# Kernel tuning notes

Hardware: AMD Instinct MI355X
Metric: run time of the kernel (lower is better)

The kernel has to match this reference:

```python
import jax, jax.numpy as jnp
import numpy as np

EMBED = 256      # input_size
DOWN = 64        # expert hidden_size
NUM_EXPERTS = 10
TOPK = 2
GATE_SCALE = 0.5
LOSS_COEF = 1.0
CV_EPS = 1e-10


def setup_inputs() -> dict:
    key = jax.random.key(0)
    ks = jax.random.split(key, 6)
    B, N = 16, 4096
    x = jax.random.normal(ks[0], (B, N, EMBED), jnp.float32)
    # gating weight (Parameter in torch; random here so top-k is non-degenerate)
    w_gate = jax.random.normal(ks[1], (EMBED, NUM_EXPERTS), jnp.float32) * 0.02
    # expert MLP params: fc1 (EMBED->DOWN), relu, fc2 (DOWN->EMBED)
    w1 = jax.random.normal(ks[2], (NUM_EXPERTS, EMBED, DOWN), jnp.float32) * (1.0 / np.sqrt(EMBED))
    b1 = jnp.zeros((NUM_EXPERTS, DOWN), jnp.float32)
    w2 = jax.random.normal(ks[3], (NUM_EXPERTS, DOWN, EMBED), jnp.float32) * (1.0 / np.sqrt(DOWN))
    b2 = jnp.zeros((NUM_EXPERTS, EMBED), jnp.float32)
    return {"x": x, "w_gate": w_gate, "w1": w1, "b1": b1, "w2": w2, "b2": b2}


def _cv_squared(v):
    # torch: x.var() / (x.mean()**2 + eps), unbiased variance
    return jnp.var(v, ddof=1) / (jnp.mean(v) ** 2 + CV_EPS)


def reference(x, w_gate, w1, b1, w2, b2):
    B, N, D = x.shape
    xt = x.reshape(B * N, D)                      # (T, D)
    T = B * N

    # --- noisy top-k gating (eval mode: no noise) ---
    logits = xt @ w_gate                          # (T, E)
    top_logits, top_idx = jax.lax.top_k(logits, TOPK)
    top_gates = jax.nn.softmax(top_logits, axis=-1)
    gates = jnp.zeros((T, NUM_EXPERTS), x.dtype).at[
        jnp.arange(T)[:, None], top_idx].set(top_gates)   # (T, E), sparse rows

    importance = gates.sum(axis=0)                               # (E,)
    load = jnp.sum(gates > 0, axis=0).astype(x.dtype)            # (E,)
    aux_loss = (_cv_squared(importance) + _cv_squared(load)) * LOSS_COEF

    # --- expert FFN dispatch+combine (dense equivalent: zero gates kill terms) ---
    h = jax.nn.relu(jnp.einsum('td,edh->teh', xt, w1) + b1[None])   # (T, E, DOWN)
    ye = jnp.einsum('teh,eho->teo', h, w2) + b2[None]               # (T, E, D)
    y = jnp.einsum('te,teo->to', gates, ye)                         # (T, D)

    out = y.reshape(B, N, -1)
    # self-KD L1 loss vs zeros, computed BEFORE gate_scale is applied
    kd_loss = jnp.mean(jnp.abs(out))
    moe_loss = aux_loss + kd_loss
    return out * GATE_SCALE, moe_loss
```

## Files before the change

### kernel.cpp

```cpp
#include <hip/hip_runtime.h>
#include <hip/hip_bf16.h>

#define T_TOKENS 65536
#define EMBED 256
#define DOWN 64
#define NE 10
#define NPAIR 100
#define MAXQ 1280
#define XROW 72

typedef __attribute__((ext_vector_type(8))) short short8;
typedef __attribute__((ext_vector_type(4))) float f32x4;

__device__ inline unsigned short f2bf(float f) {
    unsigned u = __builtin_bit_cast(unsigned, f);
    u += 0x7fff + ((u >> 16) & 1);
    return (unsigned short)(u >> 16);
}
__device__ inline float bf2f(unsigned short h) {
    unsigned u = ((unsigned)h) << 16;
    return __builtin_bit_cast(float, u);
}

__global__ __launch_bounds__(256) void pack_kernel(
    const float* __restrict__ w1, const float* __restrict__ w2,
    unsigned short* __restrict__ w1ph, unsigned short* __restrict__ w1pl,
    unsigned short* __restrict__ w2ph, unsigned short* __restrict__ w2pl)
{
    int gid = blockIdx.x * 256 + threadIdx.x;
    int lane = gid & 63;
    int fid = gid >> 6;
    int n16 = lane & 15;
    int kbase = ((lane >> 4) & 3) * 8;
    if (fid < 320) {
        int kb = fid & 7, ect = fid >> 3;
        int ct = ect & 3, e = ect >> 2;
        int n = ct * 16 + n16;
        int k0 = kb * 32 + kbase;
#pragma unroll
        for (int j = 0; j < 8; ++j) {
            float v = w1[((size_t)e * EMBED + k0 + j) * DOWN + n];
            unsigned short h = f2bf(v);
            w1ph[(size_t)fid * 512 + lane * 8 + j] = h;
            w1pl[(size_t)fid * 512 + lane * 8 + j] = f2bf(v - bf2f(h));
        }
    } else if (fid < 640) {
        int f2 = fid - 320;
        int kb = f2 & 1, ect = f2 >> 1;
        int ct = ect & 15, e = ect >> 4;
        int n = ct * 16 + n16;
        int k0 = kb * 32 + kbase;
#pragma unroll
        for (int j = 0; j < 8; ++j) {
            float v = w2[((size_t)e * DOWN + k0 + j) * EMBED + n];
            unsigned short h = f2bf(v);
            w2ph[(size_t)f2 * 512 + lane * 8 + j] = h;
            w2pl[(size_t)f2 * 512 + lane * 8 + j] = f2bf(v - bf2f(h));
        }
    }
}

__global__ __launch_bounds__(256) void gating_kernel(
    const float* __restrict__ x, const float* __restrict__ wg,
    int* __restrict__ pcount, float* __restrict__ importance,
    int* __restrict__ btok, float* __restrict__ bg0)
{
    __shared__ float Xs[2][256 * 33];
    __shared__ int lcount[NPAIR];
    __shared__ int gbase[NPAIR];
    __shared__ float limp[16];
    int tid = threadIdx.x;
    if (tid < NPAIR) lcount[tid] = 0;
    if (tid < 16) limp[tid] = 0.f;

    int tokbase = blockIdx.x * 256;
    const float4* x4 = (const float4*)x;
    int rbase = tid >> 3, c4 = tid & 7;

    float4 pre0[8], pre1[8];
#pragma unroll
    for (int i = 0; i < 8; ++i)
        pre0[i] = x4[(size_t)(tokbase + i * 32 + rbase) * 64 + c4];
#pragma unroll
    for (int i = 0; i < 8; ++i)
        pre1[i] = x4[(size_t)(tokbase + i * 32 + rbase) * 64 + 8 + c4];

    float acc[NE];
#pragma unroll
    for (int e = 0; e < NE; e++) acc[e] = 0.f;

    for (int cp = 0; cp < 4; ++cp) {
        {
            float* buf = Xs[0];
#pragma unroll
            for (int i = 0; i < 8; ++i) {
                float* d = &buf[(i * 32 + rbase) * 33 + c4 * 4];
                d[0] = pre0[i].x; d[1] = pre0[i].y; d[2] = pre0[i].z; d[3] = pre0[i].w;
            }
            if (cp < 3) {
#pragma unroll
                for (int i = 0; i < 8; ++i)
                    pre0[i] = x4[(size_t)(tokbase + i * 32 + rbase) * 64 + (2 * cp + 2) * 8 + c4];
            }
            __syncthreads();
            const float* wgc = wg + (2 * cp) * 32 * NE;
#pragma unroll
            for (int c = 0; c < 32; ++c) {
                float xv = buf[tid * 33 + c];
#pragma unroll
                for (int e = 0; e < NE; ++e)
                    acc[e] = fmaf(xv, wgc[c * NE + e], acc[e]);
            }
        }
        {
            float* buf = Xs[1];
#pragma unroll
            for (int i = 0; i < 8; ++i) {
                float* d = &buf[(i * 32 + rbase) * 33 + c4 * 4];
                d[0] = pre1[i].x; d[1] = pre1[i].y; d[2] = pre1[i].z; d[3] = pre1[i].w;
            }
            if (cp < 3) {
#pragma unroll
                for (int i = 0; i < 8; ++i)
                    pre1[i] = x4[(size_t)(tokbase + i * 32 + rbase) * 64 + (2 * cp + 3) * 8 + c4];
            }
            __syncthreads();
            const float* wgc = wg + (2 * cp + 1) * 32 * NE;
#pragma unroll
            for (int c = 0; c < 32; ++c) {
                float xv = buf[tid * 33 + c];
#pragma unroll
                for (int e = 0; e < NE; ++e)
                    acc[e] = fmaf(xv, wgc[c * NE + e], acc[e]);
            }
        }
    }

    float l0 = -INFINITY, l1 = -INFINITY;
    int i0 = 0, i1 = 0;
#pragma unroll
    for (int e = 0; e < NE; e++) {
        float v = acc[e];
        if (v > l0) { l1 = l0; i1 = i0; l0 = v; i0 = e; }
        else if (v > l1) { l1 = v; i1 = e; }
    }
    float ex = __expf(l1 - l0);
    float g0 = 1.f / (1.f + ex);

    int p = i0 * NE + i1;
    int lp = atomicAdd(&lcount[p], 1);
    atomicAdd(&limp[i0], g0);
    atomicAdd(&limp[i1], 1.f - g0);
    __syncthreads();
    if (tid < NPAIR) {
        int c = lcount[tid];
        gbase[tid] = c ? atomicAdd(&pcount[tid], c) : 0;
    }
    if (tid < NE) atomicAdd(&importance[tid], limp[tid]);
    __syncthreads();
    int pos = gbase[p] + lp;
    btok[p * T_TOKENS + pos] = tokbase + tid;
    bg0[p * T_TOKENS + pos] = g0;
}

__global__ __launch_bounds__(128) void queue_kernel(const int* __restrict__ pcount,
                             int* __restrict__ qp, int* __restrict__ qs, int* __restrict__ nq)
{
    __shared__ int sc[2][128];
    int tid = threadIdx.x;
    int c = (tid < NPAIR) ? pcount[tid] : 0;
    int t = (c + 63) >> 6;
    sc[0][tid] = t;
    __syncthreads();
    int cur = 0;
#pragma unroll
    for (int o = 1; o < 128; o <<= 1) {
        int v = sc[cur][tid] + ((tid >= o) ? sc[cur][tid - o] : 0);
        sc[cur ^ 1][tid] = v;
        __syncthreads();
        cur ^= 1;
    }
    int incl = sc[cur][tid];
    int excl = incl - t;
    if (tid == 127) *nq = incl;
    for (int i = 0; i < t; ++i) { qp[excl + i] = tid; qs[excl + i] = i * 64; }
}

__global__ __launch_bounds__(256, 3) void expert_kernel(
    const float* __restrict__ x,
    const unsigned short* __restrict__ w1ph, const unsigned short* __restrict__ w1pl,
    const unsigned short* __restrict__ w2ph, const unsigned short* __restrict__ w2pl,
    const float* __restrict__ b1, const float* __restrict__ b2,
    const int* __restrict__ pcount, const int* __restrict__ qp, const int* __restrict__ qs,
    const int* __restrict__ nq,
    const int* __restrict__ btok, const float* __restrict__ bg0,
    float* __restrict__ out, float* __restrict__ kdpart)
{
    int bid = blockIdx.x;
    if (bid >= *nq) return;
    int p = qp[bid], s = qs[bid];
    int e0 = p / NE, e1 = p - e0 * NE;
    int m = min(64, pcount[p] - s);

    __shared__ __align__(16) unsigned short Hbuf[16384];
    __shared__ int toks[64];
    __shared__ float gv0s[64], gv1s[64];
    __shared__ float kdw[4];

    unsigned short* const Xh  = Hbuf;
    unsigned short* const Xl  = Hbuf + 64 * XROW;
    unsigned short* const H0h = Hbuf;
    unsigned short* const H0l = Hbuf + 4096;
    unsigned short* const H1h = Hbuf + 8192;
    unsigned short* const H1l = Hbuf + 12288;

    int tid = threadIdx.x;
    if (tid < 64) {
        int v = 0; float g = 0.f;
        if (tid < m) {
            v = btok[p * T_TOKENS + s + tid];
            g = bg0[p * T_TOKENS + s + tid];
        }
        toks[tid] = v;
        gv0s[tid] = g;
        gv1s[tid] = (tid < m) ? (1.f - g) : 0.f;
    }
    __syncthreads();

    int lane = tid & 63, wv = tid >> 6;
    int ln15 = lane & 15, quad = lane >> 4;
    int srow = tid >> 2, sc0 = (tid & 3) * 16;
    const float* xrow = x + (size_t)toks[srow] * EMBED;
    bool srow_ok = srow < m;

    f32x4 a10[4], a11[4];
#pragma unroll
    for (int rt = 0; rt < 4; ++rt) { a10[rt] = (f32x4){0,0,0,0}; a11[rt] = (f32x4){0,0,0,0}; }

    const unsigned short* w1h0 = w1ph + (((size_t)e0 * 4 + wv) * 8) * 512;
    const unsigned short* w1l0 = w1pl + (((size_t)e0 * 4 + wv) * 8) * 512;
    const unsigned short* w1h1 = w1ph + (((size_t)e1 * 4 + wv) * 8) * 512;
    const unsigned short* w1l1 = w1pl + (((size_t)e1 * 4 + wv) * 8) * 512;

    for (int cc = 0; cc < 4; ++cc) {
#pragma unroll
        for (int p4 = 0; p4 < 4; ++p4) {
            int col = sc0 + p4 * 4;
            float4 v = make_float4(0.f, 0.f, 0.f, 0.f);
            if (srow_ok) v = *(const float4*)(xrow + cc * 64 + col);
            const float* vs = (const float*)&v;
            ushort4 hv, lv;
            unsigned short* hp = (unsigned short*)&hv;
            unsigned short* lp2 = (unsigned short*)&lv;
#pragma unroll
            for (int i = 0; i < 4; ++i) {
                unsigned short h = f2bf(vs[i]);
                hp[i] = h;
                lp2[i] = f2bf(vs[i] - bf2f(h));
            }
            *(ushort4*)&Xh[srow * XROW + col] = hv;
            *(ushort4*)&Xl[srow * XROW + col] = lv;
        }
        __syncthreads();
#pragma unroll
        for (int kb = 0; kb < 2; ++kb) {
            int kbg = cc * 2 + kb;
            short8 bh0 = *(const short8*)(w1h0 + (size_t)kbg * 512 + lane * 8);
            short8 bl0 = *(const short8*)(w1l0 + (size_t)kbg * 512 + lane * 8);
            short8 bh1 = *(const short8*)(w1h1 + (size_t)kbg * 512 + lane * 8);
            short8 bl1 = *(const short8*)(w1l1 + (size_t)kbg * 512 + lane * 8);
            int aoff = kb * 32 + quad * 8;
#pragma unroll
            for (int rt = 0; rt < 4; ++rt) {
                short8 ah = *(const short8*)&Xh[(rt * 16 + ln15) * XROW + aoff];
                short8 al = *(const short8*)&Xl[(rt * 16 + ln15) * XROW + aoff];
                a10[rt] = __builtin_amdgcn_mfma_f32_16x16x32_bf16(ah, bh0, a10[rt], 0, 0, 0);
                a10[rt] = __builtin_amdgcn_mfma_f32_16x16x32_bf16(ah, bl0, a10[rt], 0, 0, 0);
                a10[rt] = __builtin_amdgcn_mfma_f32_16x16x32_bf16(al, bh0, a10[rt], 0, 0, 0);
                a11[rt] = __builtin_amdgcn_mfma_f32_16x16x32_bf16(ah, bh1, a11[rt], 0, 0, 0);
                a11[rt] = __builtin_amdgcn_mfma_f32_16x16x32_bf16(ah, bl1, a11[rt], 0, 0, 0);
                a11[rt] = __builtin_amdgcn_mfma_f32_16x16x32_bf16(al, bh1, a11[rt], 0, 0, 0);
            }
        }
        __syncthreads();
    }

    {
        float b1v0 = b1[e0 * DOWN + wv * 16 + ln15];
        float b1v1 = b1[e1 * DOWN + wv * 16 + ln15];
        int kbH = wv >> 1;
        int laneH = (((wv & 1) * 2 + (ln15 >> 3)) * 16) + quad * 4;
        int jH = ln15 & 7;
#pragma unroll
        for (int rt = 0; rt < 4; ++rt) {
#pragma unroll
            for (int r = 0; r < 4; ++r) {
                int row = rt * 16 + quad * 4 + r;
                float g0 = gv0s[row], g1 = gv1s[row];
                float h0 = fmaxf(a10[rt][r] + b1v0, 0.f) * g0;
                float h1 = fmaxf(a11[rt][r] + b1v1, 0.f) * g1;
                int idx = ((rt * 2 + kbH) * 64 + laneH + r) * 8 + jH;
                unsigned short h0h = f2bf(h0);
                unsigned short h1h = f2bf(h1);
                H0h[idx] = h0h; H0l[idx] = f2bf(h0 - bf2f(h0h));
                H1h[idx] = h1h; H1l[idx] = f2bf(h1 - bf2f(h1h));
            }
        }
    }
    __syncthreads();

    float b20[4], b21[4];
#pragma unroll
    for (int ci = 0; ci < 4; ++ci) {
        b20[ci] = b2[e0 * EMBED + (wv * 4 + ci) * 16 + ln15];
        b21[ci] = b2[e1 * EMBED + (wv * 4 + ci) * 16 + ln15];
    }
    float kdacc = 0.f;
#pragma unroll
    for (int rt = 0; rt < 4; ++rt) {
        short8 ah0[2], al0[2], ah1[2], al1[2];
#pragma unroll
        for (int kb = 0; kb < 2; ++kb) {
            int base = ((rt * 2 + kb) * 64 + lane) * 8;
            ah0[kb] = *(const short8*)&H0h[base];
            al0[kb] = *(const short8*)&H0l[base];
            ah1[kb] = *(const short8*)&H1h[base];
            al1[kb] = *(const short8*)&H1l[base];
        }
        int rowb = rt * 16 + quad * 4;
        float gr0[4], gr1[4];
#pragma unroll
        for (int r = 0; r < 4; ++r) { gr0[r] = gv0s[rowb + r]; gr1[r] = gv1s[rowb + r]; }
#pragma unroll
        for (int ci = 0; ci < 4; ++ci) {
            int ct = wv * 4 + ci;
            const unsigned short* p0h = w2ph + (((size_t)e0 * 16 + ct) * 2) * 512;
            const unsigned short* p0l = w2pl + (((size_t)e0 * 16 + ct) * 2) * 512;
            const unsigned short* p1h = w2ph + (((size_t)e1 * 16 + ct) * 2) * 512;
            const unsigned short* p1l = w2pl + (((size_t)e1 * 16 + ct) * 2) * 512;
            f32x4 acc = (f32x4){0, 0, 0, 0};
#pragma unroll
            for (int kb = 0; kb < 2; ++kb) {
                short8 bh = *(const short8*)(p0h + kb * 512 + lane * 8);
                short8 bl = *(const short8*)(p0l + kb * 512 + lane * 8);
                acc = __builtin_amdgcn_mfma_f32_16x16x32_bf16(ah0[kb], bh, acc, 0, 0, 0);
                acc = __builtin_amdgcn_mfma_f32_16x16x32_bf16(ah0[kb], bl, acc, 0, 0, 0);
                acc = __builtin_amdgcn_mfma_f32_16x16x32_bf16(al0[kb], bh, acc, 0, 0, 0);
                short8 ch = *(const short8*)(p1h + kb * 512 + lane * 8);
                short8 cl = *(const short8*)(p1l + kb * 512 + lane * 8);
                acc = __builtin_amdgcn_mfma_f32_16x16x32_bf16(ah1[kb], ch, acc, 0, 0, 0);
                acc = __builtin_amdgcn_mfma_f32_16x16x32_bf16(ah1[kb], cl, acc, 0, 0, 0);
                acc = __builtin_amdgcn_mfma_f32_16x16x32_bf16(al1[kb], ch, acc, 0, 0, 0);
            }
#pragma unroll
            for (int r = 0; r < 4; ++r) {
                int row = rowb + r;
                float val = acc[r] + gr0[r] * b20[ci] + gr1[r] * b21[ci];
                if (row < m) {
                    kdacc += fabsf(val);
                    out[(size_t)toks[row] * EMBED + ct * 16 + ln15] = 0.5f * val;
                }
            }
        }
    }
#pragma unroll
    for (int o = 32; o > 0; o >>= 1) kdacc += __shfl_down(kdacc, o, 64);
    if (lane == 0) kdw[wv] = kdacc;
    __syncthreads();
    if (tid == 0)
        atomicAdd(&kdpart[bid & 63], kdw[0] + kdw[1] + kdw[2] + kdw[3]);
}

__global__ __launch_bounds__(128) void loss_kernel(const int* __restrict__ pcount,
                            const float* __restrict__ importance,
                            const float* __restrict__ kdpart, float* __restrict__ loss_out)
{
    __shared__ float sload[NE];
    __shared__ float simp[NE];
    __shared__ float skd;
    int tid = threadIdx.x;
    if (tid < NE) { sload[tid] = 0.f; simp[tid] = importance[tid]; }
    __syncthreads();
    if (tid < 64) {
        float kd = kdpart[tid];
#pragma unroll
        for (int o = 32; o > 0; o >>= 1) kd += __shfl_down(kd, o, 64);
        if (tid == 0) skd = kd;
    }
    if (tid < NPAIR) {
        float c = (float)pcount[tid];
        atomicAdd(&sload[tid / NE], c);
        atomicAdd(&sload[tid % NE], c);
    }
    __syncthreads();
    if (tid == 0) {
        float kd = skd * (1.f / (float)((size_t)T_TOKENS * EMBED));
        float mi = 0.f, ml = 0.f;
        for (int e = 0; e < NE; e++) { mi += simp[e]; ml += sload[e]; }
        mi *= (1.f / NE); ml *= (1.f / NE);
        float vi = 0.f, vl = 0.f;
        for (int e = 0; e < NE; e++) {
            float di = simp[e] - mi; vi += di * di;
            float dl = sload[e] - ml; vl += dl * dl;
        }
        vi *= (1.f / (NE - 1)); vl *= (1.f / (NE - 1));
        float aux = vi / (mi * mi + 1e-10f) + vl / (ml * ml + 1e-10f);
        loss_out[0] = aux + kd;
    }
}

extern "C" void kernel_launch(void* const* d_in, const int* in_sizes, int n_in,
                              void* d_out, int out_size, void* d_ws, size_t ws_size,
                              hipStream_t stream)
{
    (void)in_sizes; (void)n_in; (void)out_size; (void)ws_size;
    const float* x  = (const float*)d_in[0];
    const float* wg = (const float*)d_in[1];
    const float* w1 = (const float*)d_in[2];
    const float* b1 = (const float*)d_in[3];
    const float* w2 = (const float*)d_in[4];
    const float* b2 = (const float*)d_in[5];
    float* out = (float*)d_out;

    char* ws = (char*)d_ws;
    int*   pcount     = (int*)ws;
    float* importance = (float*)(ws + 512);
    float* kdpart     = (float*)(ws + 576);
    int*   nq         = (int*)(ws + 832);
    int*   qp         = (int*)(ws + 1024);
    int*   qs         = (int*)(ws + 1024 + MAXQ * 4);
    size_t off = 16384;
    int*   btok = (int*)(ws + off);    off += (size_t)NPAIR * T_TOKENS * 4;
    float* bg0  = (float*)(ws + off);  off += (size_t)NPAIR * T_TOKENS * 4;
    unsigned short* w1ph = (unsigned short*)(ws + off); off += 327680;
    unsigned short* w1pl = (unsigned short*)(ws + off); off += 327680;
    unsigned short* w2ph = (unsigned short*)(ws + off); off += 327680;
    unsigned short* w2pl = (unsigned short*)(ws + off); off += 327680;

    hipMemsetAsync(ws, 0, 1024, stream);

    pack_kernel<<<160, 256, 0, stream>>>(w1, w2, w1ph, w1pl, w2ph, w2pl);
    gating_kernel<<<T_TOKENS / 256, 256, 0, stream>>>(x, wg, pcount, importance, btok, bg0);
    queue_kernel<<<1, 128, 0, stream>>>(pcount, qp, qs, nq);
    expert_kernel<<<1114, 256, 0, stream>>>(
        x, w1ph, w1pl, w2ph, w2pl, b1, b2, pcount, qp, qs, nq, btok, bg0, out, kdpart);
    loss_kernel<<<1, 128, 0, stream>>>(pcount, importance, kdpart, out + (size_t)T_TOKENS * EMBED);
}
```

Baseline: 227.5 us.

## Fuse pack, gating, queue and loss kernels via last-block completion counters

Merges weight packing into the gating launch as extra blocks, and moves the queue prefix-scan into the last-finishing gating block using an atomic completion counter. The loss computation moves into the last-finishing expert block the same way, cutting five launches to two. This removes launch gaps and tiny single-block kernels, at the cost of threadfence plus atomic overhead in every block. It also adds a serial tail in the last block, and the expert grid now grows to cover more possible queues.

Result: slower. 369.4 us (+62.4%).

```diff
diff --git a/kernel.cpp b/kernel.cpp
--- a/kernel.cpp
+++ b/kernel.cpp
@@ -8,6 +8,9 @@
 #define NPAIR 100
 #define MAXQ 1280
 #define XROW 72
+#define NGATE 256
+#define NPACK 160
+#define NEXP 1123
 
 typedef __attribute__((ext_vector_type(8))) short short8;
 typedef __attribute__((ext_vector_type(4))) float f32x4;
@@ -22,54 +25,57 @@
     return __builtin_bit_cast(float, u);
 }
 
-__global__ __launch_bounds__(256) void pack_kernel(
+__global__ __launch_bounds__(256) void gate_pack_kernel(
+    const float* __restrict__ x, const float* __restrict__ wg,
     const float* __restrict__ w1, const float* __restrict__ w2,
     unsigned short* __restrict__ w1ph, unsigned short* __restrict__ w1pl,
-    unsigned short* __restrict__ w2ph, unsigned short* __restrict__ w2pl)
+    unsigned short* __restrict__ w2ph, unsigned short* __restrict__ w2pl,
+    int* __restrict__ pcount, float* __restrict__ importance,
+    int* __restrict__ btok, float* __restrict__ bg0,
+    int* __restrict__ qp, int* __restrict__ qs, int* __restrict__ nq,
+    int* __restrict__ gcount)
 {
-    int gid = blockIdx.x * 256 + threadIdx.x;
-    int lane = gid & 63;
-    int fid = gid >> 6;
-    int n16 = lane & 15;
-    int kbase = ((lane >> 4) & 3) * 8;
-    if (fid < 320) {
-        int kb = fid & 7, ect = fid >> 3;
-        int ct = ect & 3, e = ect >> 2;
-        int n = ct * 16 + n16;
-        int k0 = kb * 32 + kbase;
-#pragma unroll
-        for (int j = 0; j < 8; ++j) {
-            float v = w1[((size_t)e * EMBED + k0 + j) * DOWN + n];
-            unsigned short h = f2bf(v);
-            w1ph[(size_t)fid * 512 + lane * 8 + j] = h;
-            w1pl[(size_t)fid * 512 + lane * 8 + j] = f2bf(v - bf2f(h));
-        }
-    } else if (fid < 640) {
-        int f2 = fid - 320;
-        int kb = f2 & 1, ect = f2 >> 1;
-        int ct = ect & 15, e = ect >> 4;
-        int n = ct * 16 + n16;
-        int k0 = kb * 32 + kbase;
-#pragma unroll
-        for (int j = 0; j < 8; ++j) {
-            float v = w2[((size_t)e * DOWN + k0 + j) * EMBED + n];
-            unsigned short h = f2bf(v);
-            w2ph[(size_t)f2 * 512 + lane * 8 + j] = h;
-            w2pl[(size_t)f2 * 512 + lane * 8 + j] = f2bf(v - bf2f(h));
-        }
-    }
-}
-
-__global__ __launch_bounds__(256) void gating_kernel(
-    const float* __restrict__ x, const float* __restrict__ wg,
-    int* __restrict__ pcount, float* __restrict__ importance,
-    int* __restrict__ btok, float* __restrict__ bg0)
-{
+    int tid = threadIdx.x;
+
+    if (blockIdx.x >= NGATE) {
+        int gid = (blockIdx.x - NGATE) * 256 + tid;
+        int lane = gid & 63;
+        int fid = gid >> 6;
+        int n16 = lane & 15;
+        int kbase = ((lane >> 4) & 3) * 8;
+        if (fid < 320) {
+            int kb = fid & 7, ect = fid >> 3;
+            int ct = ect & 3, e = ect >> 2;
+            int n = ct * 16 + n16;
+            int k0 = kb * 32 + kbase;
+#pragma unroll
+            for (int j = 0; j < 8; ++j) {
+                float v = w1[((size_t)e * EMBED + k0 + j) * DOWN + n];
+                unsigned short h = f2bf(v);
+                w1ph[(size_t)fid * 512 + lane * 8 + j] = h;
+                w1pl[(size_t)fid * 512 + lane * 8 + j] = f2bf(v - bf2f(h));
+            }
+        } else if (fid < 640) {
+            int f2 = fid - 320;
+            int kb = f2 & 1, ect = f2 >> 1;
+            int ct = ect & 15, e = ect >> 4;
+            int n = ct * 16 + n16;
+            int k0 = kb * 32 + kbase;
+#pragma unroll
+            for (int j = 0; j < 8; ++j) {
+                float v = w2[((size_t)e * DOWN + k0 + j) * EMBED + n];
+                unsigned short h = f2bf(v);
+                w2ph[(size_t)f2 * 512 + lane * 8 + j] = h;
+                w2pl[(size_t)f2 * 512 + lane * 8 + j] = f2bf(v - bf2f(h));
+            }
+        }
+        return;
+    }
+
     __shared__ float Xs[2][256 * 33];
     __shared__ int lcount[NPAIR];
     __shared__ int gbase[NPAIR];
     __shared__ float limp[16];
-    int tid = threadIdx.x;
     if (tid < NPAIR) lcount[tid] = 0;
     if (tid < 16) limp[tid] = 0.f;
 
@@ -161,29 +167,30 @@
     int pos = gbase[p] + lp;
     btok[p * T_TOKENS + pos] = tokbase + tid;
     bg0[p * T_TOKENS + pos] = g0;
-}
-
-__global__ __launch_bounds__(128) void queue_kernel(const int* __restrict__ pcount,
-                             int* __restrict__ qp, int* __restrict__ qs, int* __restrict__ nq)
-{
-    __shared__ int sc[2][128];
-    int tid = threadIdx.x;
-    int c = (tid < NPAIR) ? pcount[tid] : 0;
-    int t = (c + 63) >> 6;
-    sc[0][tid] = t;
+
+    __threadfence();
+    __shared__ int qlast;
+    if (tid == 0) qlast = (atomicAdd(gcount, 1) == NGATE - 1);
     __syncthreads();
-    int cur = 0;
-#pragma unroll
-    for (int o = 1; o < 128; o <<= 1) {
-        int v = sc[cur][tid] + ((tid >= o) ? sc[cur][tid - o] : 0);
-        sc[cur ^ 1][tid] = v;
-        __syncthreads();
-        cur ^= 1;
-    }
-    int incl = sc[cur][tid];
-    int excl = incl - t;
-    if (tid == 127) *nq = incl;
-    for (int i = 0; i < t; ++i) { qp[excl + i] = tid; qs[excl + i] = i * 64; }
+    if (qlast) {
+        int* sa = (int*)&Xs[0][0];
+        int* sb = (int*)&Xs[0][256];
+        int c = (tid < NPAIR) ? atomicAdd(&pcount[tid], 0) : 0;
+        int t = (c + 63) >> 6;
+        sa[tid] = t;
+        __syncthreads();
+        int* rd = sa; int* wr = sb;
+        for (int o = 1; o < 256; o <<= 1) {
+            int v = rd[tid] + ((tid >= o) ? rd[tid - o] : 0);
+            wr[tid] = v;
+            __syncthreads();
+            int* tmp = rd; rd = wr; wr = tmp;
+        }
+        int incl = rd[tid];
+        int excl = incl - t;
+        if (tid == 255) *nq = incl;
+        for (int i = 0; i < t; ++i) { qp[excl + i] = tid; qs[excl + i] = i * 64; }
+    }
 }
 
 __global__ __launch_bounds__(256, 3) void expert_kernel(
@@ -194,14 +201,10 @@
     const int* __restrict__ pcount, const int* __restrict__ qp, const int* __restrict__ qs,
     const int* __restrict__ nq,
     const int* __restrict__ btok, const float* __restrict__ bg0,
-    float* __restrict__ out, float* __restrict__ kdpart)
+    float* __restrict__ out, float* __restrict__ kdpart,
+    const float* __restrict__ importance, int* __restrict__ ecount,
+    float* __restrict__ loss_out)
 {
-    int bid = blockIdx.x;
-    if (bid >= *nq) return;
-    int p = qp[bid], s = qs[bid];
-    int e0 = p / NE, e1 = p - e0 * NE;
-    int m = min(64, pcount[p] - s);
-
     __shared__ __align__(16) unsigned short Hbuf[16384];
     __shared__ int toks[64];
     __shared__ float gv0s[64], gv1s[64];
@@ -215,197 +218,203 @@
     unsigned short* const H1l = Hbuf + 12288;
 
     int tid = threadIdx.x;
-    if (tid < 64) {
-        int v = 0; float g = 0.f;
-        if (tid < m) {
-            v = btok[p * T_TOKENS + s + tid];
-            g = bg0[p * T_TOKENS + s + tid];
-        }
-        toks[tid] = v;
-        gv0s[tid] = g;
-        gv1s[tid] = (tid < m) ? (1.f - g) : 0.f;
-    }
+    int bid = blockIdx.x;
+    if (bid < *nq) {
+        int p = qp[bid], s = qs[bid];
+        int e0 = p / NE, e1 = p - e0 * NE;
+        int m = min(64, pcount[p] - s);
+
+        if (tid < 64) {
+            int v = 0; float g = 0.f;
+            if (tid < m) {
+                v = btok[p * T_TOKENS + s + tid];
+                g = bg0[p * T_TOKENS + s + tid];
+            }
+            toks[tid] = v;
+            gv0s[tid] = g;
+            gv1s[tid] = (tid < m) ? (1.f - g) : 0.f;
+        }
+        __syncthreads();
+
+        int lane = tid & 63, wv = tid >> 6;
+        int ln15 = lane & 15, quad = lane >> 4;
+        int srow = tid >> 2, sc0 = (tid & 3) * 16;
+        const float* xrow = x + (size_t)toks[srow] * EMBED;
+        bool srow_ok = srow < m;
+
+        f32x4 a10[4], a11[4];
+#pragma unroll
+        for (int rt = 0; rt < 4; ++rt) { a10[rt] = (f32x4){0,0,0,0}; a11[rt] = (f32x4){0,0,0,0}; }
+
+        const unsigned short* w1h0 = w1ph + (((size_t)e0 * 4 + wv) * 8) * 512;
+        const unsigned short* w1l0 = w1pl + (((size_t)e0 * 4 + wv) * 8) * 512;
+        const unsigned short* w1h1 = w1ph + (((size_t)e1 * 4 + wv) * 8) * 512;
+        const unsigned short* w1l1 = w1pl + (((size_t)e1 * 4 + wv) * 8) * 512;
+
+        for (int cc = 0; cc < 4; ++cc) {
+#pragma unroll
+            for (int p4 = 0; p4 < 4; ++p4) {
+                int col = sc0 + p4 * 4;
+                float4 v = make_float4(0.f, 0.f, 0.f, 0.f);
+                if (srow_ok) v = *(const float4*)(xrow + cc * 64 + col);
+                const float* vs = (const float*)&v;
+                ushort4 hv, lv;
+                unsigned short* hp = (unsigned short*)&hv;
+                unsigned short* lp2 = (unsigned short*)&lv;
+#pragma unroll
+                for (int i = 0; i < 4; ++i) {
+                    unsigned short h = f2bf(vs[i]);
+                    hp[i] = h;
+                    lp2[i] = f2bf(vs[i] - bf2f(h));
+                }
+                *(ushort4*)&Xh[srow * XROW + col] = hv;
+                *(ushort4*)&Xl[srow * XROW + col] = lv;
+            }
+            __syncthreads();
+#pragma unroll
+            for (int kb = 0; kb < 2; ++kb) {
+                int kbg = cc * 2 + kb;
+                short8 bh0 = *(const short8*)(w1h0 + (size_t)kbg * 512 + lane * 8);
+                short8 bl0 = *(const short8*)(w1l0 + (size_t)kbg * 512 + lane * 8);
+                short8 bh1 = *(const short8*)(w1h1 + (size_t)kbg * 512 + lane * 8);
+                short8 bl1 = *(const short8*)(w1l1 + (size_t)kbg * 512 + lane * 8);
+                int aoff = kb * 32 + quad * 8;
+#pragma unroll
+                for (int rt = 0; rt < 4; ++rt) {
+                    short8 ah = *(const short8*)&Xh[(rt * 16 + ln15) * XROW + aoff];
+                    short8 al = *(const short8*)&Xl[(rt * 16 + ln15) * XROW + aoff];
+                    a10[rt] = __builtin_amdgcn_mfma_f32_16x16x32_bf16(ah, bh0, a10[rt], 0, 0, 0);
+                    a10[rt] = __builtin_amdgcn_mfma_f32_16x16x32_bf16(ah, bl0, a10[rt], 0, 0, 0);
+                    a10[rt] = __builtin_amdgcn_mfma_f32_16x16x32_bf16(al, bh0, a10[rt], 0, 0, 0);
+                    a11[rt] = __builtin_amdgcn_mfma_f32_16x16x32_bf16(ah, bh1, a11[rt], 0, 0, 0);
+                    a11[rt] = __builtin_amdgcn_mfma_f32_16x16x32_bf16(ah, bl1, a11[rt], 0, 0, 0);
+                    a11[rt] = __builtin_amdgcn_mfma_f32_16x16x32_bf16(al, bh1, a11[rt], 0, 0, 0);
+                }
+            }
+            __syncthreads();
+        }
+
+        {
+            float b1v0 = b1[e0 * DOWN + wv * 16 + ln15];
+            float b1v1 = b1[e1 * DOWN + wv * 16 + ln15];
+            int kbH = wv >> 1;
+            int laneH = (((wv & 1) * 2 + (ln15 >> 3)) * 16) + quad * 4;
+            int jH = ln15 & 7;
+#pragma unroll
+            for (int rt = 0; rt < 4; ++rt) {
+#pragma unroll
+                for (int r = 0; r < 4; ++r) {
+                    int row = rt * 16 + quad * 4 + r;
+                    float g0 = gv0s[row], g1 = gv1s[row];
+                    float h0 = fmaxf(a10[rt][r] + b1v0, 0.f) * g0;
+                    float h1 = fmaxf(a11[rt][r] + b1v1, 0.f) * g1;
+                    int idx = ((rt * 2 + kbH) * 64 + laneH + r) * 8 + jH;
+                    unsigned short h0h = f2bf(h0);
+                    unsigned short h1h = f2bf(h1);
+                    H0h[idx] = h0h; H0l[idx] = f2bf(h0 - bf2f(h0h));
+                    H1h[idx] = h1h; H1l[idx] = f2bf(h1 - bf2f(h1h));
+                }
+            }
+        }
+        __syncthreads();
+
+        float b20[4], b21[4];
+#pragma unroll
+        for (int ci = 0; ci < 4; ++ci) {
+            b20[ci] = b2[e0 * EMBED + (wv * 4 + ci) * 16 + ln15];
+            b21[ci] = b2[e1 * EMBED + (wv * 4 + ci) * 16 + ln15];
+        }
+        float kdacc = 0.f;
+#pragma unroll
+        for (int rt = 0; rt < 4; ++rt) {
+            short8 ah0[2], al0[2], ah1[2], al1[2];
+#pragma unroll
+            for (int kb = 0; kb < 2; ++kb) {
+                int base = ((rt * 2 + kb) * 64 + lane) * 8;
+                ah0[kb] = *(const short8*)&H0h[base];
+                al0[kb] = *(const short8*)&H0l[base];
+                ah1[kb] = *(const short8*)&H1h[base];
+                al1[kb] = *(const short8*)&H1l[base];
+            }
+            int rowb = rt * 16 + quad * 4;
+            float gr0[4], gr1[4];
+#pragma unroll
+            for (int r = 0; r < 4; ++r) { gr0[r] = gv0s[rowb + r]; gr1[r] = gv1s[rowb + r]; }
+#pragma unroll
+            for (int ci = 0; ci < 4; ++ci) {
+                int ct = wv * 4 + ci;
+                const unsigned short* p0h = w2ph + (((size_t)e0 * 16 + ct) * 2) * 512;
+                const unsigned short* p0l = w2pl + (((size_t)e0 * 16 + ct) * 2) * 512;
+                const unsigned short* p1h = w2ph + (((size_t)e1 * 16 + ct) * 2) * 512;
+                const unsigned short* p1l = w2pl + (((size_t)e1 * 16 + ct) * 2) * 512;
+                f32x4 acc = (f32x4){0, 0, 0, 0};
+#pragma unroll
+                for (int kb = 0; kb < 2; ++kb) {
+                    short8 bh = *(const short8*)(p0h + kb * 512 + lane * 8);
+                    short8 bl = *(const short8*)(p0l + kb * 512 + lane * 8);
+                    acc = __builtin_amdgcn_mfma_f32_16x16x32_bf16(ah0[kb], bh, acc, 0, 0, 0);
+                    acc = __builtin_amdgcn_mfma_f32_16x16x32_bf16(ah0[kb], bl, acc, 0, 0, 0);
+                    acc = __builtin_amdgcn_mfma_f32_16x16x32_bf16(al0[kb], bh, acc, 0, 0, 0);
+                    short8 ch = *(const short8*)(p1h + kb * 512 + lane * 8);
+                    short8 cl = *(const short8*)(p1l + kb * 512 + lane * 8);
+                    acc = __builtin_amdgcn_mfma_f32_16x16x32_bf16(ah1[kb], ch, acc, 0, 0, 0);
+                    acc = __builtin_amdgcn_mfma_f32_16x16x32_bf16(ah1[kb], cl, acc, 0, 0, 0);
+                    acc = __builtin_amdgcn_mfma_f32_16x16x32_bf16(al1[kb], ch, acc, 0, 0, 0);
+                }
+#pragma unroll
+                for (int r = 0; r < 4; ++r) {
+                    int row = rowb + r;
+                    float val = acc[r] + gr0[r] * b20[ci] + gr1[r] * b21[ci];
+                    if (row < m) {
+                        kdacc += fabsf(val);
+                        out[(size_t)toks[row] * EMBED + ct * 16 + ln15] = 0.5f * val;
+                    }
+                }
+            }
+        }
+#pragma unroll
+        for (int o = 32; o > 0; o >>= 1) kdacc += __shfl_down(kdacc, o, 64);
+        if (lane == 0) kdw[tid >> 6] = kdacc;
+        __syncthreads();
+        if (tid == 0)
+            atomicAdd(&kdpart[bid & 63], kdw[0] + kdw[1] + kdw[2] + kdw[3]);
+    }
+
+    __threadfence();
+    __shared__ int elast;
+    if (tid == 0) elast = (atomicAdd(ecount, 1) == (int)gridDim.x - 1);
     __syncthreads();
-
-    int lane = tid & 63, wv = tid >> 6;
-    int ln15 = lane & 15, quad = lane >> 4;
-    int srow = tid >> 2, sc0 = (tid & 3) * 16;
-    const float* xrow = x + (size_t)toks[srow] * EMBED;
-    bool srow_ok = srow < m;
-
-    f32x4 a10[4], a11[4];
-#pragma unroll
-    for (int rt = 0; rt < 4; ++rt) { a10[rt] = (f32x4){0,0,0,0}; a11[rt] = (f32x4){0,0,0,0}; }
-
-    const unsigned short* w1h0 = w1ph + (((size_t)e0 * 4 + wv) * 8) * 512;
-    const unsigned short* w1l0 = w1pl + (((size_t)e0 * 4 + wv) * 8) * 512;
-    const unsigned short* w1h1 = w1ph + (((size_t)e1 * 4 + wv) * 8) * 512;
-    const unsigned short* w1l1 = w1pl + (((size_t)e1 * 4 + wv) * 8) * 512;
-
-    for (int cc = 0; cc < 4; ++cc) {
-#pragma unroll
-        for (int p4 = 0; p4 < 4; ++p4) {
-            int col = sc0 + p4 * 4;
-            float4 v = make_float4(0.f, 0.f, 0.f, 0.f);
-            if (srow_ok) v = *(const float4*)(xrow + cc * 64 + col);
-            const float* vs = (const float*)&v;
-            ushort4 hv, lv;
-            unsigned short* hp = (unsigned short*)&hv;
-            unsigned short* lp2 = (unsigned short*)&lv;
-#pragma unroll
-            for (int i = 0; i < 4; ++i) {
-                unsigned short h = f2bf(vs[i]);
-                hp[i] = h;
-                lp2[i] = f2bf(vs[i] - bf2f(h));
-            }
-            *(ushort4*)&Xh[srow * XROW + col] = hv;
-            *(ushort4*)&Xl[srow * XROW + col] = lv;
-        }
-        __syncthreads();
-#pragma unroll
-        for (int kb = 0; kb < 2; ++kb) {
-            int kbg = cc * 2 + kb;
-            short8 bh0 = *(const short8*)(w1h0 + (size_t)kbg * 512 + lane * 8);
-            short8 bl0 = *(const short8*)(w1l0 + (size_t)kbg * 512 + lane * 8);
-            short8 bh1 = *(const short8*)(w1h1 + (size_t)kbg * 512 + lane * 8);
-            short8 bl1 = *(const short8*)(w1l1 + (size_t)kbg * 512 + lane * 8);
-            int aoff = kb * 32 + quad * 8;
-#pragma unroll
-            for (int rt = 0; rt < 4; ++rt) {
-                short8 ah = *(const short8*)&Xh[(rt * 16 + ln15) * XROW + aoff];
-                short8 al = *(const short8*)&Xl[(rt * 16 + ln15) * XROW + aoff];
-                a10[rt] = __builtin_amdgcn_mfma_f32_16x16x32_bf16(ah, bh0, a10[rt], 0, 0, 0);
-                a10[rt] = __builtin_amdgcn_mfma_f32_16x16x32_bf16(ah, bl0, a10[rt], 0, 0, 0);
-                a10[rt] = __builtin_amdgcn_mfma_f32_16x16x32_bf16(al, bh0, a10[rt], 0, 0, 0);
-                a11[rt] = __builtin_amdgcn_mfma_f32_16x16x32_bf16(ah, bh1, a11[rt], 0, 0, 0);
-                a11[rt] = __builtin_amdgcn_mfma_f32_16x16x32_bf16(ah, bl1, a11[rt], 0, 0, 0);
-                a11[rt] = __builtin_amdgcn_mfma_f32_16x16x32_bf16(al, bh1, a11[rt], 0, 0, 0);
-            }
-        }
-        __syncthreads();
-    }
-
-    {
-        float b1v0 = b1[e0 * DOWN + wv * 16 + ln15];
-        float b1v1 = b1[e1 * DOWN + wv * 16 + ln15];
-        int kbH = wv >> 1;
-        int laneH = (((wv & 1) * 2 + (ln15 >> 3)) * 16) + quad * 4;
-        int jH = ln15 & 7;
-#pragma unroll
-        for (int rt = 0; rt < 4; ++rt) {
-#pragma unroll
-            for (int r = 0; r < 4; ++r) {
-                int row = rt * 16 + quad * 4 + r;
-                float g0 = gv0s[row], g1 = gv1s[row];
-                float h0 = fmaxf(a10[rt][r] + b1v0, 0.f) * g0;
-                float h1 = fmaxf(a11[rt][r] + b1v1, 0.f) * g1;
-                int idx = ((rt * 2 + kbH) * 64 + laneH + r) * 8 + jH;
-                unsigned short h0h = f2bf(h0);
-                unsigned short h1h = f2bf(h1);
-                H0h[idx] = h0h; H0l[idx] = f2bf(h0 - bf2f(h0h));
-                H1h[idx] = h1h; H1l[idx] = f2bf(h1 - bf2f(h1h));
-            }
-        }
-    }
-    __syncthreads();
-
-    float b20[4], b21[4];
-#pragma unroll
-    for (int ci = 0; ci < 4; ++ci) {
-        b20[ci] = b2[e0 * EMBED + (wv * 4 + ci) * 16 + ln15];
-        b21[ci] = b2[e1 * EMBED + (wv * 4 + ci) * 16 + ln15];
-    }
-    float kdacc = 0.f;
-#pragma unroll
-    for (int rt = 0; rt < 4; ++rt) {
-        short8 ah0[2], al0[2], ah1[2], al1[2];
-#pragma unroll
-        for (int kb = 0; kb < 2; ++kb) {
-            int base = ((rt * 2 + kb) * 64 + lane) * 8;
-            ah0[kb] = *(const short8*)&H0h[base];
-            al0[kb] = *(const short8*)&H0l[base];
-            ah1[kb] = *(const short8*)&H1h[base];
-            al1[kb] = *(const short8*)&H1l[base];
-        }
-        int rowb = rt * 16 + quad * 4;
-        float gr0[4], gr1[4];
-#pragma unroll
-        for (int r = 0; r < 4; ++r) { gr0[r] = gv0s[rowb + r]; gr1[r] = gv1s[rowb + r]; }
-#pragma unroll
-        for (int ci = 0; ci < 4; ++ci) {
-            int ct = wv * 4 + ci;
-            const unsigned short* p0h = w2ph + (((size_t)e0 * 16 + ct) * 2) * 512;
-            const unsigned short* p0l = w2pl + (((size_t)e0 * 16 + ct) * 2) * 512;
-            const unsigned short* p1h = w2ph + (((size_t)e1 * 16 + ct) * 2) * 512;
-            const unsigned short* p1l = w2pl + (((size_t)e1 * 16 + ct) * 2) * 512;
-            f32x4 acc = (f32x4){0, 0, 0, 0};
-#pragma unroll
-            for (int kb = 0; kb < 2; ++kb) {
-                short8 bh = *(const short8*)(p0h + kb * 512 + lane * 8);
-                short8 bl = *(const short8*)(p0l + kb * 512 + lane * 8);
-                acc = __builtin_amdgcn_mfma_f32_16x16x32_bf16(ah0[kb], bh, acc, 0, 0, 0);
-                acc = __builtin_amdgcn_mfma_f32_16x16x32_bf16(ah0[kb], bl, acc, 0, 0, 0);
-                acc = __builtin_amdgcn_mfma_f32_16x16x32_bf16(al0[kb], bh, acc, 0, 0, 0);
-                short8 ch = *(const short8*)(p1h + kb * 512 + lane * 8);
-                short8 cl = *(const short8*)(p1l + kb * 512 + lane * 8);
-                acc = __builtin_amdgcn_mfma_f32_16x16x32_bf16(ah1[kb], ch, acc, 0, 0, 0);
-                acc = __builtin_amdgcn_mfma_f32_16x16x32_bf16(ah1[kb], cl, acc, 0, 0, 0);
-                acc = __builtin_amdgcn_mfma_f32_16x16x32_bf16(al1[kb], ch, acc, 0, 0, 0);
-            }
-#pragma unroll
-            for (int r = 0; r < 4; ++r) {
-                int row = rowb + r;
-                float val = acc[r] + gr0[r] * b20[ci] + gr1[r] * b21[ci];
-                if (row < m) {
-                    kdacc += fabsf(val);
-                    out[(size_t)toks[row] * EMBED + ct * 16 + ln15] = 0.5f * val;
-                }
-            }
-        }
-    }
-#pragma unroll
-    for (int o = 32; o > 0; o >>= 1) kdacc += __shfl_down(kdacc, o, 64);
-    if (lane == 0) kdw[wv] = kdacc;
-    __syncthreads();
-    if (tid == 0)
-        atomicAdd(&kdpart[bid & 63], kdw[0] + kdw[1] + kdw[2] + kdw[3]);
-}
-
-__global__ __launch_bounds__(128) void loss_kernel(const int* __restrict__ pcount,
-                            const float* __restrict__ importance,
-                            const float* __restrict__ kdpart, float* __restrict__ loss_out)
-{
-    __shared__ float sload[NE];
-    __shared__ float simp[NE];
-    __shared__ float skd;
-    int tid = threadIdx.x;
-    if (tid < NE) { sload[tid] = 0.f; simp[tid] = importance[tid]; }
-    __syncthreads();
-    if (tid < 64) {
-        float kd = kdpart[tid];
-#pragma unroll
-        for (int o = 32; o > 0; o >>= 1) kd += __shfl_down(kd, o, 64);
-        if (tid == 0) skd = kd;
-    }
-    if (tid < NPAIR) {
-        float c = (float)pcount[tid];
-        atomicAdd(&sload[tid / NE], c);
-        atomicAdd(&sload[tid % NE], c);
-    }
-    __syncthreads();
-    if (tid == 0) {
-        float kd = skd * (1.f / (float)((size_t)T_TOKENS * EMBED));
-        float mi = 0.f, ml = 0.f;
-        for (int e = 0; e < NE; e++) { mi += simp[e]; ml += sload[e]; }
-        mi *= (1.f / NE); ml *= (1.f / NE);
-        float vi = 0.f, vl = 0.f;
-        for (int e = 0; e < NE; e++) {
-            float di = simp[e] - mi; vi += di * di;
-            float dl = sload[e] - ml; vl += dl * dl;
-        }
-        vi *= (1.f / (NE - 1)); vl *= (1.f / (NE - 1));
-        float aux = vi / (mi * mi + 1e-10f) + vl / (ml * ml + 1e-10f);
-        loss_out[0] = aux + kd;
+    if (elast) {
+        __shared__ float sload[16];
+        __shared__ float skd;
+        if (tid < 16) sload[tid] = 0.f;
+        __syncthreads();
+        if (tid < 64) {
+            float kd = atomicAdd(&kdpart[tid], 0.f);
+#pragma unroll
+            for (int o = 32; o > 0; o >>= 1) kd += __shfl_down(kd, o, 64);
+            if (tid == 0) skd = kd;
+        }
+        if (tid < NPAIR) {
+            float c = (float)pcount[tid];
+            atomicAdd(&sload[tid / NE], c);
+            atomicAdd(&sload[tid % NE], c);
+        }
+        __syncthreads();
+        if (tid == 0) {
+            float kd = skd * (1.f / (float)((size_t)T_TOKENS * EMBED));
+            float mi = 0.f, ml = 0.f;
+            for (int e = 0; e < NE; e++) { mi += importance[e]; ml += sload[e]; }
+            mi *= (1.f / NE); ml *= (1.f / NE);
+            float vi = 0.f, vl = 0.f;
+            for (int e = 0; e < NE; e++) {
+                float di = importance[e] - mi; vi += di * di;
+                float dl = sload[e] - ml; vl += dl * dl;
+            }
+            vi *= (1.f / (NE - 1)); vl *= (1.f / (NE - 1));
+            float aux = vi / (mi * mi + 1e-10f) + vl / (ml * ml + 1e-10f);
+            loss_out[0] = aux + kd;
+        }
     }
 }
 
@@ -427,6 +436,8 @@
     float* importance = (float*)(ws + 512);
     float* kdpart     = (float*)(ws + 576);
     int*   nq         = (int*)(ws + 832);
+    int*   gcount     = (int*)(ws + 840);
+    int*   ecount     = (int*)(ws + 848);
     int*   qp         = (int*)(ws + 1024);
     int*   qs         = (int*)(ws + 1024 + MAXQ * 4);
     size_t off = 16384;
@@ -439,10 +450,10 @@
 
     hipMemsetAsync(ws, 0, 1024, stream);
 
-    pack_kernel<<<160, 256, 0, stream>>>(w1, w2, w1ph, w1pl, w2ph, w2pl);
-    gating_kernel<<<T_TOKENS / 256, 256, 0, stream>>>(x, wg, pcount, importance, btok, bg0);
-    queue_kernel<<<1, 128, 0, stream>>>(pcount, qp, qs, nq);
-    expert_kernel<<<1114, 256, 0, stream>>>(
-        x, w1ph, w1pl, w2ph, w2pl, b1, b2, pcount, qp, qs, nq, btok, bg0, out, kdpart);
-    loss_kernel<<<1, 128, 0, stream>>>(pcount, importance, kdpart, out + (size_t)T_TOKENS * EMBED);
+    gate_pack_kernel<<<NGATE + NPACK, 256, 0, stream>>>(
+        x, wg, w1, w2, w1ph, w1pl, w2ph, w2pl,
+        pcount, importance, btok, bg0, qp, qs, nq, gcount);
+    expert_kernel<<<NEXP, 256, 0, stream>>>(
+        x, w1ph, w1pl, w2ph, w2pl, b1, b2, pcount, qp, qs, nq, btok, bg0, out, kdpart,
+        importance, ecount, out + (size_t)T_TOKENS * EMBED);
 }
```
